# Kernel tuning notes

Hardware: AMD Instinct MI355X
Metric: run time of the kernel (lower is better)

The kernel has to match this reference:

```python
import jax, jax.numpy as jnp
from jax import lax
import numpy as np

STRIDES = (8.0, 16.0, 32.0)
SIZES = ((256, 256), (128, 128), (64, 64))  # HxW per level for a 2048x2048 input
C = 80            # num_classes
TOPK = 1000       # topk_candidates per level
CONF = 0.05       # conf_thresh
NMS_T = 0.6       # nms_thresh
OFFSET = 1.0e5    # class offset for multiclass (class-aware) NMS


def _anchors(H, W, stride):
    ys, xs = jnp.meshgrid(jnp.arange(H, dtype=jnp.float32),
                          jnp.arange(W, dtype=jnp.float32), indexing='ij')
    a = jnp.stack([xs, ys], axis=-1).reshape(-1, 2)  # [M,2] (x,y)
    return (a + 0.5) * stride


def _level(obj, cls, reg, H, W, stride):
    # decode boxes: ctr = reg[:, :2]*s + anchor; wh = exp(reg[:, 2:])*s
    anc = _anchors(H, W, stride)
    ctr = reg[:, :2] * stride + anc
    wh = jnp.exp(reg[:, 2:]) * stride
    boxes = jnp.concatenate([ctr - 0.5 * wh, ctr + 0.5 * wh], axis=-1)  # [M,4]
    # fused score: sqrt(sigmoid(obj) * sigmoid(cls)), flattened over (M, C)
    scores = jnp.sqrt(jax.nn.sigmoid(obj) * jax.nn.sigmoid(cls)).reshape(-1)  # [M*C]
    k = min(TOPK, boxes.shape[0])
    top_scores, top_idx = lax.top_k(scores, k)  # == sort(desc)[:k]
    anchor_idx = top_idx // C
    labels = top_idx % C
    return boxes[anchor_idx], top_scores, labels


def _iou_matrix(b):
    x1, y1, x2, y2 = b[:, 0], b[:, 1], b[:, 2], b[:, 3]
    area = jnp.maximum(x2 - x1, 0.0) * jnp.maximum(y2 - y1, 0.0)
    xx1 = jnp.maximum(x1[:, None], x1[None, :])
    yy1 = jnp.maximum(y1[:, None], y1[None, :])
    xx2 = jnp.minimum(x2[:, None], x2[None, :])
    yy2 = jnp.minimum(y2[:, None], y2[None, :])
    inter = jnp.maximum(xx2 - xx1, 0.0) * jnp.maximum(yy2 - yy1, 0.0)
    return inter / (area[:, None] + area[None, :] - inter + 1e-10)


def setup_inputs() -> dict:
    key = jax.random.key(0)
    ks = jax.random.split(key, 9)
    inp = {}
    names = ['obj0', 'cls0', 'reg0', 'obj1', 'cls1', 'reg1', 'obj2', 'cls2', 'reg2']
    shapes = [(65536, 1), (65536, C), (65536, 4),
              (16384, 1), (16384, C), (16384, 4),
              (4096, 1), (4096, C), (4096, 4)]
    for n, s, k in zip(names, shapes, ks):
        inp[n] = jax.random.normal(k, s, dtype=jnp.float32)
    return inp


def reference(obj0, cls0, reg0, obj1, cls1, reg1, obj2, cls2, reg2):
    levels = [(obj0, cls0, reg0), (obj1, cls1, reg1), (obj2, cls2, reg2)]
    bs, ss, ls = [], [], []
    for (o, c, r), (H, W), s in zip(levels, SIZES, STRIDES):
        b, sc, lb = _level(o, c, r, H, W, s)
        bs.append(b); ss.append(sc); ls.append(lb)
    boxes = jnp.concatenate(bs, axis=0)   # [N,4], N = 3*TOPK
    scores = jnp.concatenate(ss, axis=0)  # [N]
    labels = jnp.concatenate(ls, axis=0)  # [N] int

    # global sort by score desc (NMS order)
    order = jnp.argsort(-scores)
    b = boxes[order]; sc = scores[order]; lb = labels[order]

    # class-aware NMS via per-class coordinate offset
    b_off = b + (lb.astype(jnp.float32) * OFFSET)[:, None]
    iou = _iou_matrix(b_off)  # [N,N]

    N = sc.shape[0]
    idx = jnp.arange(N)
    keep0 = sc > CONF  # conf_thresh gating; below-thresh never suppress

    def body(i, keep):
        sup = (iou[i] > NMS_T) & (idx > i) & keep[i]
        return keep & (~sup)

    keep = lax.fori_loop(0, N, body, keep0)
    # fixed-shape outputs: suppressed / below-threshold detections get score 0
    return b, jnp.where(keep, sc, 0.0), lb
```

## Files before the change

kernel.cpp:

```cpp
#include <hip/hip_runtime.h>
#include <cstdint>
#include <math.h>

#define C_CLS      80
#define TOPK       1000
#define NCAND      3000
#define OFFSET_F   100000.0f
#define FLOOR_BITS 0x3F333333u
#define NBINS      512
#define CAP        8192
#define MASK_W     48
#define NBLK       47
#define RTILE      2048
#define ITILE      16
#define CAPB0      57344
#define CAPB1      49152
#define CAPB2      32768
#define FBIN0      154u
#define FBIN1      103u
#define FBIN2      52u
#define STGB       1024
#define SLICE      375

static __device__ __forceinline__ float np_expf(float x) {
    const float magic = 12582912.0f;
    float q = fmaf(x, 1.442695040888963407359924681e+00f, magic);
    q = q - magic;
    float r = fmaf(q, -6.93145752e-1f, x);
    r = fmaf(q, -1.428606765330187045e-06f, r);
    float p = fmaf(r, 5.082762527590693718096e-04f, 6.757896990527504603057e-03f);
    p = fmaf(p, r, 5.114512081637298353406e-02f);
    p = fmaf(p, r, 2.473615434895520810817e-01f);
    p = fmaf(p, r, 7.257664613233124478488e-01f);
    p = fmaf(p, r, 9.999999999980870924916e-01f);
    float d = fmaf(r, 2.159509375685829852307e-02f, -2.742335390411667452936e-01f);
    d = fmaf(d, r, 1.0f);
    float e = p / d;
    int qi = (int)q;
    return __uint_as_float(__float_as_uint(e) + ((unsigned int)qi << 23));
}

static __device__ __forceinline__ float sigmoid_np(float x) {
    float e = np_expf(-x);
    return 1.0f / (1.0f + e);
}

__global__ void sweep_kernel(const float* __restrict__ c0, const float* __restrict__ c1,
                             const float* __restrict__ c2,
                             const float* __restrict__ o0, const float* __restrict__ o1,
                             const float* __restrict__ o2,
                             unsigned int* __restrict__ hist, unsigned int* __restrict__ meta,
                             unsigned long long* __restrict__ buf_all) {
    __shared__ unsigned int h[NBINS];
    __shared__ unsigned long long stg[STGB];
    __shared__ float s_sig[112], s_flo[112];
    __shared__ unsigned int scnt, srb;

    int bb = blockIdx.x;
    const float *cls, *obj; int base, lvl;
    if (bb < 640)      { lvl = 0; cls = c0; obj = o0; base = bb * 8192; }
    else if (bb < 800) { lvl = 1; cls = c1; obj = o1; base = (bb - 640) * 8192; }
    else               { lvl = 2; cls = c2; obj = o2; base = (bb - 800) * 8192; }
    const unsigned int fbin = (lvl == 0) ? FBIN0 : (lvl == 1) ? FBIN1 : FBIN2;
    const unsigned int Fb   = FLOOR_BITS + (fbin << 14);
    unsigned long long* buf = buf_all + ((lvl == 0) ? 0 : (lvl == 1) ? CAPB0 : (CAPB0 + CAPB1));
    const unsigned int capl = (lvl == 0) ? CAPB0 : (lvl == 1) ? CAPB1 : CAPB2;
    unsigned int* mcnt = &meta[lvl * 4];

    float4 cv[8];
    #pragma unroll
    for (int it = 0; it < 8; ++it)
        cv[it] = *(const float4*)(cls + base + it * 1024 + threadIdx.x * 4);

    for (int i = threadIdx.x; i < NBINS; i += 256) h[i] = 0;
    if (threadIdx.x == 0) scnt = 0;
    int a0 = base / C_CLS;
    int nA = (base + 8191) / C_CLS - a0 + 1;
    float F2f = __uint_as_float(Fb); F2f = F2f * F2f;
    if (threadIdx.x < nA) {
        float sig = sigmoid_np(obj[a0 + threadIdx.x]);
        s_sig[threadIdx.x] = sig;
        float q = F2f / fmaxf(sig, 1e-30f);
        s_flo[threadIdx.x] = (q >= 0.9999f) ? 9.18f : (__logf(q / (1.0f - q)) - 0.03f);
    }
    __syncthreads();

    #pragma unroll
    for (int it = 0; it < 8; ++it) {
        int e = base + it * 1024 + threadIdx.x * 4;
        int ai0 = e / C_CLS;
        int r0  = e - ai0 * C_CLS;
        ai0 -= a0;
        float c4[4] = {cv[it].x, cv[it].y, cv[it].z, cv[it].w};
        #pragma unroll
        for (int k = 0; k < 4; ++k) {
            int ai = ai0 + ((r0 + k) >= C_CLS ? 1 : 0);
            float c = c4[k];
            if (c >= s_flo[ai]) {
                float s = sqrtf(s_sig[ai] * sigmoid_np(c));
                unsigned int bits = __float_as_uint(s);
                if (bits >= Fb) {
                    int ee = e + k;
                    atomicAdd(&h[(bits - FLOOR_BITS) >> 14], 1u);
                    unsigned long long key = ((unsigned long long)bits << 32) |
                                             (unsigned long long)(0xFFFFFFFFu - (unsigned int)ee);
                    unsigned int pos = atomicAdd(&scnt, 1u);
                    if (pos < STGB) stg[pos] = key;
                    else {
                        unsigned int gp = atomicAdd(mcnt, 1u);
                        if (gp < capl) buf[gp] = key;
                    }
                }
            }
        }
    }
    __syncthreads();
    unsigned int n = scnt; if (n > STGB) n = STGB;
    if (threadIdx.x == 0 && n) srb = atomicAdd(mcnt, n);
    __syncthreads();
    if (n) {
        unsigned int rb = srb;
        for (unsigned int i = threadIdx.x; i < n; i += 256) {
            unsigned int dst = rb + i;
            if (dst < capl) buf[dst] = stg[i];
        }
    }
    unsigned int* ho = hist + lvl * NBINS;
    for (int i = threadIdx.x; i < NBINS; i += 256)
        if (h[i]) atomicAdd(&ho[i], h[i]);
}

__global__ void collectB_kernel(const unsigned long long* __restrict__ buf_all,
                                const unsigned int* __restrict__ hist,
                                unsigned int* __restrict__ meta,
                                unsigned long long* __restrict__ cand_all) {
    __shared__ unsigned int sh[NBINS];
    __shared__ unsigned int sT;
    int lvl = blockIdx.y;
    for (int i = threadIdx.x; i < NBINS; i += 256) sh[i] = hist[lvl * NBINS + i];
    __syncthreads();
    if (threadIdx.x == 0) {
        unsigned int cum = 0; int B = 0;
        for (int b = 320; b >= 0; --b) {
            cum += sh[b];
            if (cum >= TOPK) { B = b; break; }
        }
        sT = FLOOR_BITS + ((unsigned int)B << 14);
    }
    __syncthreads();
    const unsigned int T = sT;
    const unsigned long long* buf = buf_all + ((lvl == 0) ? 0 : (lvl == 1) ? CAPB0 : (CAPB0 + CAPB1));
    unsigned int capl = (lvl == 0) ? CAPB0 : (lvl == 1) ? CAPB1 : CAPB2;
    unsigned int m = meta[lvl * 4]; if (m > capl) m = capl;
    unsigned long long* cand = cand_all + (size_t)lvl * CAP;
    for (unsigned int i = blockIdx.x * 256 + threadIdx.x; i < m; i += 16 * 256) {
        unsigned long long e = buf[i];
        if ((unsigned int)(e >> 32) >= T) {
            unsigned int pos = atomicAdd(&meta[lvl * 4 + 1], 1u);
            if (pos < CAP) cand[pos] = e;
        }
    }
}

__global__ void rank_kernel(const unsigned long long* __restrict__ cand_all,
                            const unsigned int* __restrict__ meta,
                            float* __restrict__ sel_score, unsigned int* __restrict__ sel_anchor,
                            unsigned int* __restrict__ sel_label) {
    __shared__ unsigned long long tile[RTILE];
    int lvl = blockIdx.y;
    const unsigned long long* cand = cand_all + (size_t)lvl * CAP;
    unsigned int m = meta[lvl * 4 + 1]; if (m > CAP) m = CAP;
    if ((unsigned int)(blockIdx.x * 256) >= m) return;
    int t = blockIdx.x * 256 + threadIdx.x;
    bool live = (unsigned int)t < m;
    unsigned long long key = live ? cand[t] : 0ull;
    int r = 0;
    for (unsigned int base = 0; base < m; base += RTILE) {
        unsigned int n = m - base; if (n > RTILE) n = RTILE;
        __syncthreads();
        for (unsigned int i = threadIdx.x; i < n; i += 256) tile[i] = cand[base + i];
        __syncthreads();
        if (live) {
            #pragma unroll 8
            for (unsigned int j = 0; j < n; ++j) r += (tile[j] > key);
        }
    }
    if (live && r < TOPK) {
        unsigned int bits = (unsigned int)(key >> 32);
        unsigned int ee   = 0xFFFFFFFFu - (unsigned int)key;
        int slot = lvl * TOPK + r;
        sel_score[slot]  = __uint_as_float(bits);
        sel_anchor[slot] = ee / C_CLS;
        sel_label[slot]  = ee % C_CLS;
    }
}

__global__ void build_sort_kernel(const float* __restrict__ reg0, const float* __restrict__ reg1,
                                  const float* __restrict__ reg2,
                                  const float* __restrict__ sel_score,
                                  const unsigned int* __restrict__ sel_anchor,
                                  const unsigned int* __restrict__ sel_label,
                                  float* __restrict__ out, float* __restrict__ sc_sorted,
                                  float* __restrict__ boff) {
    __shared__ unsigned long long keys[NCAND];
    for (int i = threadIdx.x; i < NCAND; i += 256) {
        unsigned int b = __float_as_uint(sel_score[i]);
        keys[i] = ((unsigned long long)b << 12) | (unsigned int)(4095 - i);
    }
    __syncthreads();
    const int gl = threadIdx.x >> 3;
    const int s  = threadIdx.x & 7;
    const int g  = blockIdx.x * 32 + gl;
    if (g >= NCAND) return;
    const unsigned long long kg = keys[g];
    int r = 0;
    const int j0 = s * SLICE;
    #pragma unroll 8
    for (int i = 0; i < SLICE; ++i) r += (keys[j0 + i] > kg);
    r += __shfl_down(r, 4, 8);
    r += __shfl_down(r, 2, 8);
    r += __shfl_down(r, 1, 8);
    if (s != 0) return;
    int lvl = g / TOPK;
    unsigned int a   = sel_anchor[g];
    unsigned int lab = sel_label[g];
    const float* reg = (lvl == 0) ? reg0 : (lvl == 1) ? reg1 : reg2;
    int   W      = (lvl == 0) ? 256 : (lvl == 1) ? 128 : 64;
    float stride = (lvl == 0) ? 8.0f : (lvl == 1) ? 16.0f : 32.0f;
    float4 rv = *(const float4*)(reg + (size_t)a * 4);
    float ax = ((float)(a % W) + 0.5f) * stride;
    float ay = ((float)(a / W) + 0.5f) * stride;
    float cx = rv.x * stride + ax;
    float cy = rv.y * stride + ay;
    float wx = np_expf(rv.z) * stride;
    float wy = np_expf(rv.w) * stride;
    float x1 = cx - 0.5f * wx, y1 = cy - 0.5f * wy;
    float x2 = cx + 0.5f * wx, y2 = cy + 0.5f * wy;
    out[r * 4 + 0] = x1; out[r * 4 + 1] = y1; out[r * 4 + 2] = x2; out[r * 4 + 3] = y2;
    sc_sorted[r] = sel_score[g];
    out[15000 + r] = (float)lab;
    float off = (float)lab * OFFSET_F;
    boff[r * 4 + 0] = x1 + off; boff[r * 4 + 1] = y1 + off;
    boff[r * 4 + 2] = x2 + off; boff[r * 4 + 3] = y2 + off;
}

__global__ void mask_kernel(const float* __restrict__ boff, unsigned long long* __restrict__ mask,
                            unsigned long long* __restrict__ diag,
                            unsigned long long* __restrict__ rnz) {
    #pragma clang fp contract(off)
    __shared__ float4 bis[ITILE];
    int i0 = blockIdx.y * ITILE;
    if (threadIdx.x < ITILE) {
        int ir = i0 + threadIdx.x; if (ir >= NCAND) ir = NCAND - 1;
        bis[threadIdx.x] = *(const float4*)(boff + (size_t)ir * 4);
    }
    __syncthreads();
    int j = blockIdx.x * 256 + threadIdx.x;
    float4 bj = {0, 0, 0, 0};
    if (j < NCAND) bj = *(const float4*)(boff + (size_t)j * 4);
    float aj = fmaxf(bj.z - bj.x, 0.0f) * fmaxf(bj.w - bj.y, 0.0f);
    int wslot = blockIdx.x * 4 + (threadIdx.x >> 6);
    #pragma unroll
    for (int ii = 0; ii < ITILE; ++ii) {
        int i = i0 + ii;
        float4 bi = bis[ii];
        bool pred = false;
        if (j < NCAND && j > i) {
            float ai = fmaxf(bi.z - bi.x, 0.0f) * fmaxf(bi.w - bi.y, 0.0f);
            float xx1 = fmaxf(bi.x, bj.x);
            float yy1 = fmaxf(bi.y, bj.y);
            float xx2 = fminf(bi.z, bj.z);
            float yy2 = fminf(bi.w, bj.w);
            float inter = fmaxf(xx2 - xx1, 0.0f) * fmaxf(yy2 - yy1, 0.0f);
            float u = ai + aj;
            u = u - inter;
            u = u + 1e-10f;
            float iou = inter / u;
            pred = (double)iou > 0.6;
        }
        unsigned long long bal = __ballot(pred);
        if ((threadIdx.x & 63) == 0 && i < NCAND) {
            mask[(size_t)i * MASK_W + wslot] = bal;
            if (wslot == (i >> 6)) diag[i] = bal;
            if (bal) atomicOr(&rnz[i >> 6], 1ull << (i & 63));
        }
    }
}

__global__ void __launch_bounds__(64) nms_reduce(const unsigned long long* __restrict__ mask,
                                                 const unsigned long long* __restrict__ diag,
                                                 const unsigned long long* __restrict__ rnzmap,
                                                 const float* __restrict__ sc,
                                                 float* __restrict__ out_sc) {
    int t = threadIdx.x;
    unsigned long long confw = 0ull;
    if (t < NBLK) {
        #pragma unroll 8
        for (int j = 0; j < 64; ++j) {
            int g = t * 64 + j;
            if (g < NCAND && (double)sc[g] > 0.05) confw |= 1ull << j;
        }
    }
    unsigned long long rnz_t = (t < NBLK) ? rnzmap[t] : 0ull;
    unsigned long long supp = 0ull, keepw = 0ull;
    unsigned long long Dcur  = diag[t];
    unsigned long long Dnext = diag[64 + t];
    for (int b = 0; b < NBLK; ++b) {
        unsigned long long Dfut = (b + 2 < NBLK) ? diag[(size_t)(b + 2) * 64 + t] : 0ull;
        unsigned long long confb = __shfl(confw, b);
        unsigned long long suppb = __shfl(supp, b);
        unsigned long long rnzb  = __shfl(rnz_t, b);
        unsigned long long res = confb & ~suppb;
        unsigned long long work = res & rnzb;
        while (work) {
            int k = __builtin_ctzll(work);
            res &= ~__shfl(Dcur, k);
            work = res & rnzb & ((k == 63) ? 0ull : (~0ull << (k + 1)));
        }
        if (t == b) keepw = res;
        unsigned long long app = res & rnzb;
        while (app) {
            int k = __builtin_ctzll(app);
            app &= app - 1;
            if (t < MASK_W) supp |= mask[(size_t)(64 * b + k) * MASK_W + t];
        }
        Dcur = Dnext; Dnext = Dfut;
    }
    if (t < NBLK) {
        #pragma unroll 8
        for (int j = 0; j < 64; ++j) {
            int g = t * 64 + j;
            if (g < NCAND) out_sc[g] = ((keepw >> j) & 1ull) ? sc[g] : 0.0f;
        }
    }
}

extern "C" void kernel_launch(void* const* d_in, const int* in_sizes, int n_in,
                              void* d_out, int out_size, void* d_ws, size_t ws_size,
                              hipStream_t stream) {
    const float* o0 = (const float*)d_in[0];
    const float* c0 = (const float*)d_in[1];
    const float* r0 = (const float*)d_in[2];
    const float* o1 = (const float*)d_in[3];
    const float* c1 = (const float*)d_in[4];
    const float* r1 = (const float*)d_in[5];
    const float* o2 = (const float*)d_in[6];
    const float* c2 = (const float*)d_in[7];
    const float* r2 = (const float*)d_in[8];
    float* out = (float*)d_out;
    char*  ws  = (char*)d_ws;

    unsigned int*       hist       = (unsigned int*)(ws + 0);
    unsigned long long* rnz        = (unsigned long long*)(ws + 6144);
    unsigned int*       meta       = (unsigned int*)(ws + 6528);
    unsigned long long* cand       = (unsigned long long*)(ws + 6592);
    float*              sel_score  = (float*)(ws + 203200);
    unsigned int*       sel_anchor = (unsigned int*)(ws + 215200);
    unsigned int*       sel_label  = (unsigned int*)(ws + 227200);
    float*              sc_sorted  = (float*)(ws + 239200);
    float*              boff       = (float*)(ws + 251200);
    unsigned long long* mask       = (unsigned long long*)(ws + 299200);
    unsigned long long* diag       = (unsigned long long*)(ws + 1454272);
    unsigned long long* fbuf       = (unsigned long long*)(ws + 299200);

    hipMemsetAsync(hist, 0, 6592, stream);

    sweep_kernel<<<840, 256, 0, stream>>>(c0, c1, c2, o0, o1, o2, hist, meta, fbuf);

    collectB_kernel<<<dim3(16, 3), 256, 0, stream>>>(fbuf, hist, meta, cand);

    rank_kernel<<<dim3(CAP / 256, 3), 256, 0, stream>>>(cand, meta, sel_score, sel_anchor, sel_label);

    build_sort_kernel<<<94, 256, 0, stream>>>(r0, r1, r2, sel_score, sel_anchor, sel_label,
                                              out, sc_sorted, boff);

    mask_kernel<<<dim3(12, 188), 256, 0, stream>>>(boff, mask, diag, rnz);

    nms_reduce<<<1, 64, 0, stream>>>(mask, diag, rnz, sc_sorted, out + 12000);
}
```

Measured before the change: 190.2 us.

## Split rank counting across 8 threads per key and coalesce NMS score I/O

The rank kernel now gives each candidate key 8 threads that stride through the shared tile and combine partial counts with shuffles, which multiplies the number of blocks by 8 and shortens each thread's serial loop. The collect kernel doubles its grid, and the mask kernel's row tile is doubled, which halves its grid in y. The single-wave NMS reduce now loads scores coalesced into registers, builds the confidence words with ballots, and writes outputs coalesced instead of each lane looping over 64 consecutive elements. The cost is more redundant tile loads across rank blocks and higher register use in nms_reduce.

```diff
diff --git a/kernel.cpp b/kernel.cpp
--- a/kernel.cpp
+++ b/kernel.cpp
@@ -12,7 +12,7 @@
 #define MASK_W     48
 #define NBLK       47
 #define RTILE      2048
-#define ITILE      16
+#define ITILE      32
 #define CAPB0      57344
 #define CAPB1      49152
 #define CAPB2      32768
@@ -153,7 +153,7 @@
     unsigned int capl = (lvl == 0) ? CAPB0 : (lvl == 1) ? CAPB1 : CAPB2;
     unsigned int m = meta[lvl * 4]; if (m > capl) m = capl;
     unsigned long long* cand = cand_all + (size_t)lvl * CAP;
-    for (unsigned int i = blockIdx.x * 256 + threadIdx.x; i < m; i += 16 * 256) {
+    for (unsigned int i = blockIdx.x * 256 + threadIdx.x; i < m; i += 32 * 256) {
         unsigned long long e = buf[i];
         if ((unsigned int)(e >> 32) >= T) {
             unsigned int pos = atomicAdd(&meta[lvl * 4 + 1], 1u);
@@ -170,8 +170,10 @@
     int lvl = blockIdx.y;
     const unsigned long long* cand = cand_all + (size_t)lvl * CAP;
     unsigned int m = meta[lvl * 4 + 1]; if (m > CAP) m = CAP;
-    if ((unsigned int)(blockIdx.x * 256) >= m) return;
-    int t = blockIdx.x * 256 + threadIdx.x;
+    if ((unsigned int)(blockIdx.x * 32) >= m) return;
+    const int gl = threadIdx.x >> 3;
+    const int s  = threadIdx.x & 7;
+    int t = blockIdx.x * 32 + gl;
     bool live = (unsigned int)t < m;
     unsigned long long key = live ? cand[t] : 0ull;
     int r = 0;
@@ -181,11 +183,13 @@
         for (unsigned int i = threadIdx.x; i < n; i += 256) tile[i] = cand[base + i];
         __syncthreads();
         if (live) {
-            #pragma unroll 8
-            for (unsigned int j = 0; j < n; ++j) r += (tile[j] > key);
-        }
-    }
-    if (live && r < TOPK) {
+            for (unsigned int j = s; j < n; j += 8) r += (tile[j] > key);
+        }
+    }
+    r += __shfl_down(r, 4, 8);
+    r += __shfl_down(r, 2, 8);
+    r += __shfl_down(r, 1, 8);
+    if (live && s == 0 && r < TOPK) {
         unsigned int bits = (unsigned int)(key >> 32);
         unsigned int ee   = 0xFFFFFFFFu - (unsigned int)key;
         int slot = lvl * TOPK + r;
@@ -293,13 +297,17 @@
                                                  const float* __restrict__ sc,
                                                  float* __restrict__ out_sc) {
     int t = threadIdx.x;
+    float scv[NBLK];
+    #pragma unroll
+    for (int w = 0; w < NBLK; ++w) {
+        int g = w * 64 + t;
+        scv[w] = (g < NCAND) ? sc[g] : 0.0f;
+    }
     unsigned long long confw = 0ull;
-    if (t < NBLK) {
-        #pragma unroll 8
-        for (int j = 0; j < 64; ++j) {
-            int g = t * 64 + j;
-            if (g < NCAND && (double)sc[g] > 0.05) confw |= 1ull << j;
-        }
+    #pragma unroll 8
+    for (int w = 0; w < NBLK; ++w) {
+        unsigned long long bal = __ballot((double)scv[w] > 0.05);
+        if (t == w) confw = bal;
     }
     unsigned long long rnz_t = (t < NBLK) ? rnzmap[t] : 0ull;
     unsigned long long supp = 0ull, keepw = 0ull;
@@ -326,12 +334,11 @@
         }
         Dcur = Dnext; Dnext = Dfut;
     }
-    if (t < NBLK) {
-        #pragma unroll 8
-        for (int j = 0; j < 64; ++j) {
-            int g = t * 64 + j;
-            if (g < NCAND) out_sc[g] = ((keepw >> j) & 1ull) ? sc[g] : 0.0f;
-        }
+    #pragma unroll 8
+    for (int w = 0; w < NBLK; ++w) {
+        unsigned long long kw = __shfl(keepw, w);
+        int g = w * 64 + t;
+        if (g < NCAND) out_sc[g] = ((kw >> t) & 1ull) ? scv[w] : 0.0f;
     }
 }
 
@@ -367,14 +374,14 @@
 
     sweep_kernel<<<840, 256, 0, stream>>>(c0, c1, c2, o0, o1, o2, hist, meta, fbuf);
 
-    collectB_kernel<<<dim3(16, 3), 256, 0, stream>>>(fbuf, hist, meta, cand);
-
-    rank_kernel<<<dim3(CAP / 256, 3), 256, 0, stream>>>(cand, meta, sel_score, sel_anchor, sel_label);
+    collectB_kernel<<<dim3(32, 3), 256, 0, stream>>>(fbuf, hist, meta, cand);
+
+    rank_kernel<<<dim3(CAP / 32, 3), 256, 0, stream>>>(cand, meta, sel_score, sel_anchor, sel_label);
 
     build_sort_kernel<<<94, 256, 0, stream>>>(r0, r1, r2, sel_score, sel_anchor, sel_label,
                                               out, sc_sorted, boff);
 
-    mask_kernel<<<dim3(12, 188), 256, 0, stream>>>(boff, mask, diag, rnz);
+    mask_kernel<<<dim3(12, 94), 256, 0, stream>>>(boff, mask, diag, rnz);
 
     nms_reduce<<<1, 64, 0, stream>>>(mask, diag, rnz, sc_sorted, out + 12000);
 }
```

Result: faster. 172.3 us (-9.4%).
